# Performance work log

Measured on AMD Instinct MI355X. Metric: run time of the kernel, lower is better.

Reference implementation:

```python
import jax, jax.numpy as jnp
import numpy as np

N = 10000      # nodes
E = 160000     # edges
F_IN = 128     # input_feature
G = 64         # graphs in batch
NC = 10        # num_classes
H1, H2, H3 = 1000, 700, 200


def _xavier(k, fi, fo):
    lim = float(np.sqrt(6.0 / (fi + fo)))
    return jax.random.uniform(k, (fi, fo), jnp.float32, -lim, lim)


def setup_inputs() -> dict:
    key = jax.random.key(0)
    ks = jax.random.split(key, 8)
    x = jax.random.normal(ks[0], (N, F_IN), jnp.float32)
    edge_index = jax.random.randint(ks[1], (2, E), 0, N)
    batch = jnp.sort(jax.random.randint(ks[2], (N,), 0, G))
    return {
        "x": x,
        "edge_index": edge_index,
        "batch": batch,
        "W1": _xavier(ks[3], F_IN, H1), "b1": jnp.zeros((H1,), jnp.float32),
        "W2": _xavier(ks[4], H1, H2),   "b2": jnp.zeros((H2,), jnp.float32),
        "W3": _xavier(ks[5], H2, H3),   "b3": jnp.zeros((H3,), jnp.float32),
        "Wl": _xavier(ks[6], H3, NC),   "bl": jnp.zeros((NC,), jnp.float32),
    }


def _gcn_conv(x, W, b, src, dst, dinv):
    # GCNConv: h = xW; out_i = sum_{j->i} d_j^-1/2 d_i^-1/2 h_j + d_i^-1 h_i + b
    h = x @ W
    coef = dinv[src] * dinv[dst]                      # [E]
    agg = jax.ops.segment_sum(h[src] * coef[:, None], dst, num_segments=N)
    agg = agg + h * (dinv * dinv)[:, None]            # self-loop term
    return agg + b


def reference(x, edge_index, batch, W1, b1, W2, b2, W3, b3, Wl, bl):
    src, dst = edge_index[0], edge_index[1]
    # degree with self-loops (edge weight 1), computed on target nodes
    deg = jax.ops.segment_sum(jnp.ones((E,), x.dtype), dst, num_segments=N) + 1.0
    dinv = jax.lax.rsqrt(deg)

    h = jax.nn.relu(_gcn_conv(x, W1, b1, src, dst, dinv))
    h = jax.nn.relu(_gcn_conv(h, W2, b2, src, dst, dinv))
    h = jax.nn.relu(_gcn_conv(h, W3, b3, src, dst, dinv))

    # global_mean_pool over graph ids
    s = jax.ops.segment_sum(h, batch, num_segments=G)
    cnt = jax.ops.segment_sum(jnp.ones((N,), h.dtype), batch, num_segments=G)
    pooled = s / jnp.maximum(cnt, 1.0)[:, None]

    # dropout is identity in eval mode
    return pooled @ Wl + bl
```

## Files before the change

### kernel.cpp

```cpp
#include <hip/hip_runtime.h>
#include <hip/hip_bf16.h>
#include <stdint.h>


#define SLOT 64

__device__ __forceinline__ uint16_t f2b(float f) {
    union { float f; uint32_t u; } v; v.f = f;
    return (uint16_t)((v.u + 0x7fffu + ((v.u >> 16) & 1u)) >> 16);
}
__device__ __forceinline__ float blo(uint32_t u) { union { uint32_t u; float f; } v; v.u = u << 16; return v.f; }
__device__ __forceinline__ float bhi(uint32_t u) { union { uint32_t u; float f; } v; v.u = u & 0xffff0000u; return v.f; }

__global__ void k_scatter(const int* __restrict__ src, const int* __restrict__ dst,
                          int* __restrict__ cursor, int* __restrict__ slots, int E) {
    int e = blockIdx.x * blockDim.x + threadIdx.x;
    if (e < E) {
        int s = src[e], d = dst[e];
        int pos = atomicAdd(&cursor[d], 1);
        if (pos < SLOT) slots[d * SLOT + pos] = s;
    }
}

__global__ void k_prep(const float* __restrict__ W1, const float* __restrict__ W2,
                       const float* __restrict__ W3,
                       uint16_t* __restrict__ T1, uint16_t* __restrict__ T2,
                       uint16_t* __restrict__ T3,
                       const float* __restrict__ b1, const float* __restrict__ b2,
                       const float* __restrict__ b3,
                       float* __restrict__ p1, float* __restrict__ p2,
                       float* __restrict__ p3,
                       const float* __restrict__ x, uint16_t* __restrict__ xb,
                       const int* __restrict__ deg, float* __restrict__ dinv,
                       int N, int F, int H1, int H2, int H3,
                       int Fp, int H1p, int H2p, int H3p, int n8) {
    __shared__ float tile[32][33];
    int z = blockIdx.z;
    if (z < 3) {
        const float* W; uint16_t* T; int K, Nn, Kp, Np;
        if (z == 0)      { W = W1; T = T1; K = F;  Nn = H1; Kp = Fp;  Np = H1p; }
        else if (z == 1) { W = W2; T = T2; K = H1; Nn = H2; Kp = H1p; Np = H2p; }
        else             { W = W3; T = T3; K = H2; Nn = H3; Kp = H2p; Np = H3p; }
        if ((int)blockIdx.x * 32 >= Kp || (int)blockIdx.y * 32 >= Np) return;
        int k0 = blockIdx.x * 32, n0 = blockIdx.y * 32;
        int tx = threadIdx.x, ty = threadIdx.y;
        for (int i = ty; i < 32; i += 8) {
            int k = k0 + i, n = n0 + tx;
            tile[i][tx] = (k < K && n < Nn) ? W[(size_t)k * Nn + n] : 0.f;
        }
        __syncthreads();
        for (int i = ty; i < 32; i += 8) {
            int n = n0 + i, k = k0 + tx;
            T[(size_t)n * Kp + k] = f2b(tile[tx][i]);
        }
    } else {
        int id = (blockIdx.y * gridDim.x + blockIdx.x) * 256 + threadIdx.y * 32 + threadIdx.x;
        if (z == 3) {
            if (id < H1p) p1[id] = (id < H1) ? b1[id] : 0.f;
            else if (id < H1p + H2p) { int k = id - H1p; p2[k] = (k < H2) ? b2[k] : 0.f; }
            else if (id < H1p + H2p + H3p) { int k = id - H1p - H2p; p3[k] = (k < H3) ? b3[k] : 0.f; }
        } else if (z == 4) {
            if (id < n8) {
                const float4* x4 = (const float4*)x;
                float4 a = x4[2 * id], b = x4[2 * id + 1];
                uint4 o;
                o.x = (uint32_t)f2b(a.x) | ((uint32_t)f2b(a.y) << 16);
                o.y = (uint32_t)f2b(a.z) | ((uint32_t)f2b(a.w) << 16);
                o.z = (uint32_t)f2b(b.x) | ((uint32_t)f2b(b.y) << 16);
                o.w = (uint32_t)f2b(b.z) | ((uint32_t)f2b(b.w) << 16);
                ((uint4*)xb)[id] = o;
            }
        } else {
            if (id < N) dinv[id] = rsqrtf((float)deg[id] + 1.0f);
        }
    }
}

__global__ __launch_bounds__(256) void k_agg_panel(
    const uint16_t* __restrict__ in, uint16_t* __restrict__ out,
    const int* __restrict__ deg_, const int* __restrict__ slots,
    const float* __restrict__ dinv, const float* __restrict__ bias,
    int N, int Hc, int HcReal, int padWrite, int pc, int P, int relu) {
    int slotg = blockIdx.x & 7;
    int panel = slotg % P;
    int seg   = slotg / P;
    int nseg  = 8 / P;
    int segLen = (N + nseg - 1) / nseg;
    int wave = threadIdx.x >> 6, lane = threadIdx.x & 63;
    int half = lane >> 5, sub = lane & 31;
    int item = (blockIdx.x >> 3) * 128 + wave * 32 + sub;
    int rel = item / pc;
    if (rel >= segLen) return;
    int node = seg * segLen + rel;
    if (node >= N) return;
    int j = panel * pc + (item - rel * pc);
    if (j >= HcReal) {
        if (padWrite && half == 0)
            ((uint4*)out)[(size_t)node * Hc + j] = (uint4){0u, 0u, 0u, 0u};
        return;
    }
    int deg = deg_[node];
    if (deg > SLOT) deg = SLOT;
    int base = node * SLOT;
    float dv = dinv[node];
    const uint4* in4 = (const uint4*)in;
    float a[8] = {0.f, 0.f, 0.f, 0.f, 0.f, 0.f, 0.f, 0.f};
    if (half == 0) {
        float self = dv * dv;
        uint4 v = in4[(size_t)node * Hc + j];
        a[0] = self * blo(v.x); a[1] = self * bhi(v.x);
        a[2] = self * blo(v.y); a[3] = self * bhi(v.y);
        a[4] = self * blo(v.z); a[5] = self * bhi(v.z);
        a[6] = self * blo(v.w); a[7] = self * bhi(v.w);
    }
    int D8 = deg & ~7;
    int e = 4 * half;
    if (e < D8) {
        int4 q = *(const int4*)&slots[base + e];
        uint4 h0 = in4[(size_t)q.x * Hc + j];
        uint4 h1 = in4[(size_t)q.y * Hc + j];
        uint4 h2 = in4[(size_t)q.z * Hc + j];
        uint4 h3 = in4[(size_t)q.w * Hc + j];
        float c0 = dinv[q.x] * dv, c1 = dinv[q.y] * dv;
        float c2 = dinv[q.z] * dv, c3 = dinv[q.w] * dv;
        for (e += 8; e < D8; e += 8) {
            int4 qn = *(const int4*)&slots[base + e];
            uint4 g0 = in4[(size_t)qn.x * Hc + j];
            uint4 g1 = in4[(size_t)qn.y * Hc + j];
            uint4 g2 = in4[(size_t)qn.z * Hc + j];
            uint4 g3 = in4[(size_t)qn.w * Hc + j];
            float d0 = dinv[qn.x] * dv, d1 = dinv[qn.y] * dv;
            float d2 = dinv[qn.z] * dv, d3 = dinv[qn.w] * dv;
            a[0] += c0 * blo(h0.x); a[1] += c0 * bhi(h0.x);
            a[2] += c0 * blo(h0.y); a[3] += c0 * bhi(h0.y);
            a[4] += c0 * blo(h0.z); a[5] += c0 * bhi(h0.z);
            a[6] += c0 * blo(h0.w); a[7] += c0 * bhi(h0.w);
            a[0] += c1 * blo(h1.x); a[1] += c1 * bhi(h1.x);
            a[2] += c1 * blo(h1.y); a[3] += c1 * bhi(h1.y);
            a[4] += c1 * blo(h1.z); a[5] += c1 * bhi(h1.z);
            a[6] += c1 * blo(h1.w); a[7] += c1 * bhi(h1.w);
            a[0] += c2 * blo(h2.x); a[1] += c2 * bhi(h2.x);
            a[2] += c2 * blo(h2.y); a[3] += c2 * bhi(h2.y);
            a[4] += c2 * blo(h2.z); a[5] += c2 * bhi(h2.z);
            a[6] += c2 * blo(h2.w); a[7] += c2 * bhi(h2.w);
            a[0] += c3 * blo(h3.x); a[1] += c3 * bhi(h3.x);
            a[2] += c3 * blo(h3.y); a[3] += c3 * bhi(h3.y);
            a[4] += c3 * blo(h3.z); a[5] += c3 * bhi(h3.z);
            a[6] += c3 * blo(h3.w); a[7] += c3 * bhi(h3.w);
            h0 = g0; h1 = g1; h2 = g2; h3 = g3;
            c0 = d0; c1 = d1; c2 = d2; c3 = d3;
        }
        a[0] += c0 * blo(h0.x); a[1] += c0 * bhi(h0.x);
        a[2] += c0 * blo(h0.y); a[3] += c0 * bhi(h0.y);
        a[4] += c0 * blo(h0.z); a[5] += c0 * bhi(h0.z);
        a[6] += c0 * blo(h0.w); a[7] += c0 * bhi(h0.w);
        a[0] += c1 * blo(h1.x); a[1] += c1 * bhi(h1.x);
        a[2] += c1 * blo(h1.y); a[3] += c1 * bhi(h1.y);
        a[4] += c1 * blo(h1.z); a[5] += c1 * bhi(h1.z);
        a[6] += c1 * blo(h1.w); a[7] += c1 * bhi(h1.w);
        a[0] += c2 * blo(h2.x); a[1] += c2 * bhi(h2.x);
        a[2] += c2 * blo(h2.y); a[3] += c2 * bhi(h2.y);
        a[4] += c2 * blo(h2.z); a[5] += c2 * bhi(h2.z);
        a[6] += c2 * blo(h2.w); a[7] += c2 * bhi(h2.w);
        a[0] += c3 * blo(h3.x); a[1] += c3 * bhi(h3.x);
        a[2] += c3 * blo(h3.y); a[3] += c3 * bhi(h3.y);
        a[4] += c3 * blo(h3.z); a[5] += c3 * bhi(h3.z);
        a[6] += c3 * blo(h3.w); a[7] += c3 * bhi(h3.w);
    }
    int t0 = half ? (D8 + 4 < deg ? D8 + 4 : deg) : D8;
    int t1 = half ? deg : (D8 + 4 < deg ? D8 + 4 : deg);
    for (int ee = t0; ee < t1; ++ee) {
        int s0 = slots[base + ee];
        uint4 h = in4[(size_t)s0 * Hc + j];
        float c = dinv[s0] * dv;
        a[0] += c * blo(h.x); a[1] += c * bhi(h.x);
        a[2] += c * blo(h.y); a[3] += c * bhi(h.y);
        a[4] += c * blo(h.z); a[5] += c * bhi(h.z);
        a[6] += c * blo(h.w); a[7] += c * bhi(h.w);
    }
#pragma unroll
    for (int t = 0; t < 8; ++t) a[t] += __shfl_xor(a[t], 32, 64);
    if (half == 0) {
        if (bias) {
            const float4* b4 = (const float4*)bias;
            float4 b0 = b4[2 * j], b1 = b4[2 * j + 1];
            a[0] += b0.x; a[1] += b0.y; a[2] += b0.z; a[3] += b0.w;
            a[4] += b1.x; a[5] += b1.y; a[6] += b1.z; a[7] += b1.w;
        }
        if (relu) {
#pragma unroll
            for (int t = 0; t < 8; ++t) a[t] = fmaxf(a[t], 0.f);
        }
        uint4 o;
        o.x = (uint32_t)f2b(a[0]) | ((uint32_t)f2b(a[1]) << 16);
        o.y = (uint32_t)f2b(a[2]) | ((uint32_t)f2b(a[3]) << 16);
        o.z = (uint32_t)f2b(a[4]) | ((uint32_t)f2b(a[5]) << 16);
        o.w = (uint32_t)f2b(a[6]) | ((uint32_t)f2b(a[7]) << 16);
        ((uint4*)out)[(size_t)node * Hc + j] = o;
    }
}

__global__ __launch_bounds__(256) void k_pool_fast(
    const uint16_t* __restrict__ h, const int* __restrict__ batch,
    float* __restrict__ pooled_sum, int N, int H, int Hp) {
    int j    = threadIdx.x & 63;
    int slot = threadIdx.x >> 6;
    int Hc   = H >> 2;
    if (j >= Hc) return;
    int HcP  = Hp >> 2;
    const uint2* h2 = (const uint2*)h;
    int base = (blockIdx.x * 4 + slot) * 16;
    float a0 = 0.f, a1 = 0.f, a2 = 0.f, a3 = 0.f;
    int gcur = -1;
#pragma unroll 4
    for (int t = 0; t < 16; ++t) {
        int node = base + t;
        if (node < N) {
            int g = batch[node];
            if (g != gcur) {
                if (gcur >= 0) {
                    float* ps = &pooled_sum[(size_t)gcur * H + j * 4];
                    atomicAdd(&ps[0], a0); atomicAdd(&ps[1], a1);
                    atomicAdd(&ps[2], a2); atomicAdd(&ps[3], a3);
                }
                gcur = g; a0 = a1 = a2 = a3 = 0.f;
            }
            uint2 v = h2[(size_t)node * HcP + j];
            a0 += blo(v.x); a1 += bhi(v.x);
            a2 += blo(v.y); a3 += bhi(v.y);
        }
    }
    if (gcur >= 0) {
        float* ps = &pooled_sum[(size_t)gcur * H + j * 4];
        atomicAdd(&ps[0], a0); atomicAdd(&ps[1], a1);
        atomicAdd(&ps[2], a2); atomicAdd(&ps[3], a3);
    }
}

typedef __attribute__((ext_vector_type(8))) short short8;
typedef __attribute__((ext_vector_type(4))) float floatx4;

#define LDSP(p) ((__attribute__((address_space(3))) void*)(uintptr_t)(p))
#define GLBP(p) ((const __attribute__((address_space(1))) void*)(uintptr_t)(p))

__global__ __launch_bounds__(256) void k_gemm128(
    const uint16_t* __restrict__ A, const uint16_t* __restrict__ Bt,
    const float* __restrict__ bias, uint16_t* __restrict__ Cout,
    int M, int Kp, int Np, int relu, int nrg, int nr) {
    int bid = blockIdx.x;
    int rsub = bid & 7;
    int t_ = bid >> 3;
    int rg = t_ % nrg, cc = t_ / nrg;
    int rt = rg * 8 + rsub;
    if (rt >= nr) return;
    int row0 = rt * 128, col0 = cc * 128;

    __shared__ uint16_t As[128 * 64];
    __shared__ uint16_t Bs[128 * 64];
    int tid = threadIdx.x;
    int wave = tid >> 6, lane = tid & 63;
    int quad = lane >> 4, m16 = lane & 15;
    int wr = wave >> 1, wc = wave & 1;

    int rA = tid >> 3;
    int cA = (tid & 7) ^ (rA & 7);
    const uint16_t* gA = A  + (size_t)(row0 + rA) * Kp + cA * 8;
    const uint16_t* gB = Bt + (size_t)(col0 + rA) * Kp + cA * 8;
    uint16_t* lA = As + tid * 8;
    uint16_t* lB = Bs + tid * 8;
    size_t rowStep32 = (size_t)32 * Kp;

    floatx4 acc[4][4];
#pragma unroll
    for (int i = 0; i < 4; ++i)
#pragma unroll
        for (int j = 0; j < 4; ++j) acc[i][j] = (floatx4){0.f, 0.f, 0.f, 0.f};

    const short* Ash = (const short*)As;
    const short* Bsh = (const short*)Bs;
    int swA = m16 & 7;

    for (int k0 = 0; k0 < Kp; k0 += 64) {
#pragma unroll
        for (int p = 0; p < 4; ++p) {
            __builtin_amdgcn_global_load_lds(GLBP(gA + p * rowStep32), LDSP(lA + p * 2048), 16, 0, 0);
            __builtin_amdgcn_global_load_lds(GLBP(gB + p * rowStep32), LDSP(lB + p * 2048), 16, 0, 0);
        }
        gA += 64; gB += 64;
        __syncthreads();
#pragma unroll
        for (int h = 0; h < 2; ++h) {
            short8 af[4], bf[4];
            int c = h * 4 + quad;
            int pos = (c ^ swA) * 8;
#pragma unroll
            for (int i = 0; i < 4; ++i)
                af[i] = *(const short8*)&Ash[(wr * 64 + i * 16 + m16) * 64 + pos];
#pragma unroll
            for (int j = 0; j < 4; ++j)
                bf[j] = *(const short8*)&Bsh[(wc * 64 + j * 16 + m16) * 64 + pos];
#pragma unroll
            for (int i = 0; i < 4; ++i)
#pragma unroll
                for (int j = 0; j < 4; ++j)
                    acc[i][j] = __builtin_amdgcn_mfma_f32_16x16x32_bf16(af[i], bf[j], acc[i][j], 0, 0, 0);
        }
        __syncthreads();
    }

    float bv[4];
#pragma unroll
    for (int j = 0; j < 4; ++j) {
        int n = col0 + wc * 64 + j * 16 + m16;
        bv[j] = bias ? bias[n] : 0.f;
    }
#pragma unroll
    for (int i = 0; i < 4; ++i) {
        int mBase = row0 + wr * 64 + i * 16 + quad * 4;
#pragma unroll
        for (int r = 0; r < 4; ++r) {
            int m = mBase + r;
            if (m < M) {
#pragma unroll
                for (int j = 0; j < 4; ++j) {
                    int n = col0 + wc * 64 + j * 16 + m16;
                    float v = acc[i][j][r] + bv[j];
                    if (relu) v = fmaxf(v, 0.f);
                    Cout[(size_t)m * Np + n] = f2b(v);
                }
            }
        }
    }
}

__global__ __launch_bounds__(256) void k_gemm64(
    const uint16_t* __restrict__ A, const uint16_t* __restrict__ Bt,
    const float* __restrict__ bias, uint16_t* __restrict__ Cout,
    int M, int Kp, int Np, int relu, int nrg, int nr) {
    int bid = blockIdx.x;
    int rsub = bid & 7;
    int t_ = bid >> 3;
    int rg = t_ % nrg, cc = t_ / nrg;
    int rt = rg * 8 + rsub;
    if (rt >= nr) return;
    int row0 = rt * 128, col0 = cc * 64;

    __shared__ uint16_t As[128 * 64];
    __shared__ uint16_t Bs[64 * 64];
    int tid = threadIdx.x;
    int wave = tid >> 6, lane = tid & 63;
    int quad = lane >> 4, m16 = lane & 15;
    int wr = wave >> 1, wc = wave & 1;

    int rA = tid >> 3;
    int cA = (tid & 7) ^ (rA & 7);
    const uint16_t* gA = A  + (size_t)(row0 + rA) * Kp + cA * 8;
    const uint16_t* gB = Bt + (size_t)(col0 + rA) * Kp + cA * 8;
    uint16_t* lA = As + tid * 8;
    uint16_t* lB = Bs + tid * 8;
    size_t rowStep32 = (size_t)32 * Kp;

    floatx4 acc[4][2];
#pragma unroll
    for (int i = 0; i < 4; ++i)
#pragma unroll
        for (int j = 0; j < 2; ++j) acc[i][j] = (floatx4){0.f, 0.f, 0.f, 0.f};

    const short* Ash = (const short*)As;
    const short* Bsh = (const short*)Bs;
    int swA = m16 & 7;

    for (int k0 = 0; k0 < Kp; k0 += 64) {
#pragma unroll
        for (int p = 0; p < 4; ++p)
            __builtin_amdgcn_global_load_lds(GLBP(gA + p * rowStep32), LDSP(lA + p * 2048), 16, 0, 0);
#pragma unroll
        for (int p = 0; p < 2; ++p)
            __builtin_amdgcn_global_load_lds(GLBP(gB + p * rowStep32), LDSP(lB + p * 2048), 16, 0, 0);
        gA += 64; gB += 64;
        __syncthreads();
#pragma unroll
        for (int h = 0; h < 2; ++h) {
            short8 af[4], bf[2];
            int c = h * 4 + quad;
            int pos = (c ^ swA) * 8;
#pragma unroll
            for (int i = 0; i < 4; ++i)
                af[i] = *(const short8*)&Ash[(wr * 64 + i * 16 + m16) * 64 + pos];
#pragma unroll
            for (int j = 0; j < 2; ++j)
                bf[j] = *(const short8*)&Bsh[(wc * 32 + j * 16 + m16) * 64 + pos];
#pragma unroll
            for (int i = 0; i < 4; ++i)
#pragma unroll
                for (int j = 0; j < 2; ++j)
                    acc[i][j] = __builtin_amdgcn_mfma_f32_16x16x32_bf16(af[i], bf[j], acc[i][j], 0, 0, 0);
        }
        __syncthreads();
    }

    float bv[2];
#pragma unroll
    for (int j = 0; j < 2; ++j) {
        int n = col0 + wc * 32 + j * 16 + m16;
        bv[j] = bias ? bias[n] : 0.f;
    }
#pragma unroll
    for (int i = 0; i < 4; ++i) {
        int mBase = row0 + wr * 64 + i * 16 + quad * 4;
#pragma unroll
        for (int r = 0; r < 4; ++r) {
            int m = mBase + r;
            if (m < M) {
#pragma unroll
                for (int j = 0; j < 2; ++j) {
                    int n = col0 + wc * 32 + j * 16 + m16;
                    float v = acc[i][j][r] + bv[j];
                    if (relu) v = fmaxf(v, 0.f);
                    Cout[(size_t)m * Np + n] = f2b(v);
                }
            }
        }
    }
}

__global__ void k_classifier(const float* __restrict__ pooled_sum,
                             const int* __restrict__ batch,
                             const float* __restrict__ Wl, const float* __restrict__ bl,
                             float* __restrict__ out, int N, int H, int NC) {
    int g = blockIdx.x, c = threadIdx.x;
    int lo = 0, hi = N;
    while (lo < hi) { int mid = (lo + hi) >> 1; if (batch[mid] < g) lo = mid + 1; else hi = mid; }
    int start = lo;
    lo = start; hi = N;
    while (lo < hi) { int mid = (lo + hi) >> 1; if (batch[mid] < g + 1) lo = mid + 1; else hi = mid; }
    int end = lo;
    float scale = 1.0f / fmaxf((float)(end - start), 1.0f);
    if (c < NC) {
        float acc = 0.f;
        for (int k = 0; k < H; ++k) acc += pooled_sum[(size_t)g * H + k] * Wl[(size_t)k * NC + c];
        out[(size_t)g * NC + c] = acc * scale + bl[c];
    }
}

static inline size_t align256(size_t x) { return (x + 255) & ~(size_t)255; }
static inline int pad128(int x) { return (x + 127) & ~127; }

extern "C" void kernel_launch(void* const* d_in, const int* in_sizes, int n_in,
                              void* d_out, int out_size, void* d_ws, size_t ws_size,
                              hipStream_t stream) {
    const float* x   = (const float*)d_in[0];
    const int*   ei  = (const int*)d_in[1];
    const int*   bat = (const int*)d_in[2];
    const float* W1  = (const float*)d_in[3];
    const float* b1  = (const float*)d_in[4];
    const float* W2  = (const float*)d_in[5];
    const float* b2  = (const float*)d_in[6];
    const float* W3  = (const float*)d_in[7];
    const float* b3  = (const float*)d_in[8];
    const float* Wl  = (const float*)d_in[9];
    const float* bl  = (const float*)d_in[10];

    const int N  = in_sizes[2];
    const int E  = in_sizes[1] / 2;
    const int F  = in_sizes[0] / N;
    const int H1 = in_sizes[4];
    const int H2 = in_sizes[6];
    const int H3 = in_sizes[8];
    const int NC = in_sizes[10];
    const int G  = out_size / NC;
    const int* src = ei;
    const int* dst = ei + E;

    const int Mp  = pad128(N);
    const int Fp  = F;
    const int H1p = pad128(H1);
    const int H2p = pad128(H2);
    const int H3p = pad128(H3);
    const int Hc2real = (H2 + 7) / 8;
    const int Hc3real = (H3 + 7) / 8;

    char* p = (char*)d_ws;
    size_t off = 0;
    auto carve = [&](size_t bytes) { void* q = p + off; off += align256(bytes); return q; };
    uint16_t* xb     = (uint16_t*)carve((size_t)Mp * Fp * 2);
    uint16_t* bufA   = (uint16_t*)carve((size_t)Mp * 2048);
    uint16_t* bufB   = (uint16_t*)carve((size_t)Mp * 2048);
    uint16_t* W1t    = (uint16_t*)carve((size_t)H1p * Fp * 2);
    uint16_t* W2t    = (uint16_t*)carve((size_t)H2p * H1p * 2);
    uint16_t* W3t    = (uint16_t*)carve((size_t)H3p * H2p * 2);
    float* b1p       = (float*)carve((size_t)H1p * 4);
    float* b2p       = (float*)carve((size_t)H2p * 4);
    float* b3p       = (float*)carve((size_t)H3p * 4);
    float* dinv      = (float*)carve((size_t)N * 4);
    int*   cursor    = (int*)carve((size_t)N * 4);
    float* pooled    = (float*)carve((size_t)G * H3 * 4);
    int*   slots     = (int*)carve((size_t)N * SLOT * 4);
    (void)ws_size;

    const int nbE = (E + 255) / 256;

    size_t zlen = (size_t)((char*)pooled - (char*)cursor) + (size_t)G * H3 * 4;
    hipMemsetAsync(cursor, 0, zlen, stream);

    k_scatter<<<nbE, 256, 0, stream>>>(src, dst, cursor, slots, E);

    k_prep<<<dim3(32, 32, 6), dim3(32, 8), 0, stream>>>(
        W1, W2, W3, W1t, W2t, W3t, b1, b2, b3, b1p, b2p, b3p, x, xb,
        cursor, dinv, N, F, H1, H2, H3, Fp, H1p, H2p, H3p, N * F / 8);

    auto agg_grid = [&](int P, int pc) {
        int nseg = 8 / P;
        int segLen = (N + nseg - 1) / nseg;
        return 8 * ((segLen * pc + 127) / 128);
    };

    const int nr  = Mp / 128;
    const int nrg = (nr + 7) / 8;

    k_agg_panel<<<agg_grid(1, 16), 256, 0, stream>>>(
        xb, bufA, cursor, slots, dinv, nullptr, N, 16, 16, 0, 16, 1, 0);
    k_gemm128<<<nrg * 8 * (H1p / 128), 256, 0, stream>>>(
        bufA, W1t, b1p, bufB, N, Fp, H1p, 1, nrg, nr);

    k_gemm128<<<nrg * 8 * (H2p / 128), 256, 0, stream>>>(
        bufB, W2t, nullptr, bufA, N, H1p, H2p, 0, nrg, nr);
    k_agg_panel<<<agg_grid(8, 12), 256, 0, stream>>>(
        bufA, bufB, cursor, slots, dinv, b2p, N, 96, Hc2real, 1, 12, 8, 1);

    k_gemm64<<<nrg * 8 * (H3p / 64), 256, 0, stream>>>(
        bufB, W3t, nullptr, bufA, N, H2p, H3p, 0, nrg, nr);
    k_agg_panel<<<agg_grid(4, 8), 256, 0, stream>>>(
        bufA, bufB, cursor, slots, dinv, b3p, N, 32, Hc3real, 0, 8, 4, 1);

    k_pool_fast<<<(N + 63) / 64, 256, 0, stream>>>(
        (const uint16_t*)bufB, bat, pooled, N, H3, H3p);
    k_classifier<<<G, 64, 0, stream>>>(pooled, bat, Wl, bl, (float*)d_out, N, H3, NC);
}
```

Before: 238.5 us.

## Fold edge scatter into prep kernel, compute dinv inline, fuse pool with classifier

Moves the edge-scatter pass into the z-slice of the prep kernel that previously computed dinv. The aggregation kernels now recompute the normalization coefficient with rsqrtf from the degree counts, so the separate dinv array is gone. Pooling and the classifier are merged through a last-block-done atomic counter. Together these remove two kernel launches and one dependency pass. The cost is extra rsqrt work per edge and a serial classifier tail that runs in a single block.

Result: slower. 308.2 us (+29.2%).

```diff
diff --git a/kernel.cpp b/kernel.cpp
--- a/kernel.cpp
+++ b/kernel.cpp
@@ -11,16 +11,6 @@
 }
 __device__ __forceinline__ float blo(uint32_t u) { union { uint32_t u; float f; } v; v.u = u << 16; return v.f; }
 __device__ __forceinline__ float bhi(uint32_t u) { union { uint32_t u; float f; } v; v.u = u & 0xffff0000u; return v.f; }
-
-__global__ void k_scatter(const int* __restrict__ src, const int* __restrict__ dst,
-                          int* __restrict__ cursor, int* __restrict__ slots, int E) {
-    int e = blockIdx.x * blockDim.x + threadIdx.x;
-    if (e < E) {
-        int s = src[e], d = dst[e];
-        int pos = atomicAdd(&cursor[d], 1);
-        if (pos < SLOT) slots[d * SLOT + pos] = s;
-    }
-}
 
 __global__ void k_prep(const float* __restrict__ W1, const float* __restrict__ W2,
                        const float* __restrict__ W3,
@@ -31,8 +21,9 @@
                        float* __restrict__ p1, float* __restrict__ p2,
                        float* __restrict__ p3,
                        const float* __restrict__ x, uint16_t* __restrict__ xb,
-                       const int* __restrict__ deg, float* __restrict__ dinv,
-                       int N, int F, int H1, int H2, int H3,
+                       const int* __restrict__ src, const int* __restrict__ dst,
+                       int* __restrict__ cursor, int* __restrict__ slots, int E,
+                       int F, int H1, int H2, int H3,
                        int Fp, int H1p, int H2p, int H3p, int n8) {
     __shared__ float tile[32][33];
     int z = blockIdx.z;
@@ -71,15 +62,19 @@
                 ((uint4*)xb)[id] = o;
             }
         } else {
-            if (id < N) dinv[id] = rsqrtf((float)deg[id] + 1.0f);
+            if (id < E) {
+                int s = src[id], d = dst[id];
+                int pos = atomicAdd(&cursor[d], 1);
+                if (pos < SLOT) slots[d * SLOT + pos] = s;
+            }
         }
     }
 }
 
 __global__ __launch_bounds__(256) void k_agg_panel(
     const uint16_t* __restrict__ in, uint16_t* __restrict__ out,
-    const int* __restrict__ deg_, const int* __restrict__ slots,
-    const float* __restrict__ dinv, const float* __restrict__ bias,
+    const int* __restrict__ degt, const int* __restrict__ slots,
+    const float* __restrict__ bias,
     int N, int Hc, int HcReal, int padWrite, int pc, int P, int relu) {
     int slotg = blockIdx.x & 7;
     int panel = slotg % P;
@@ -99,14 +94,14 @@
             ((uint4*)out)[(size_t)node * Hc + j] = (uint4){0u, 0u, 0u, 0u};
         return;
     }
-    int deg = deg_[node];
-    if (deg > SLOT) deg = SLOT;
+    int degFull = degt[node];
+    int deg = degFull > SLOT ? SLOT : degFull;
     int base = node * SLOT;
-    float dv = dinv[node];
+    float ndf = (float)(degFull + 1);
     const uint4* in4 = (const uint4*)in;
     float a[8] = {0.f, 0.f, 0.f, 0.f, 0.f, 0.f, 0.f, 0.f};
     if (half == 0) {
-        float self = dv * dv;
+        float self = 1.0f / ndf;
         uint4 v = in4[(size_t)node * Hc + j];
         a[0] = self * blo(v.x); a[1] = self * bhi(v.x);
         a[2] = self * blo(v.y); a[3] = self * bhi(v.y);
@@ -121,16 +116,20 @@
         uint4 h1 = in4[(size_t)q.y * Hc + j];
         uint4 h2 = in4[(size_t)q.z * Hc + j];
         uint4 h3 = in4[(size_t)q.w * Hc + j];
-        float c0 = dinv[q.x] * dv, c1 = dinv[q.y] * dv;
-        float c2 = dinv[q.z] * dv, c3 = dinv[q.w] * dv;
+        float c0 = rsqrtf(ndf * (float)(degt[q.x] + 1));
+        float c1 = rsqrtf(ndf * (float)(degt[q.y] + 1));
+        float c2 = rsqrtf(ndf * (float)(degt[q.z] + 1));
+        float c3 = rsqrtf(ndf * (float)(degt[q.w] + 1));
         for (e += 8; e < D8; e += 8) {
             int4 qn = *(const int4*)&slots[base + e];
             uint4 g0 = in4[(size_t)qn.x * Hc + j];
             uint4 g1 = in4[(size_t)qn.y * Hc + j];
             uint4 g2 = in4[(size_t)qn.z * Hc + j];
             uint4 g3 = in4[(size_t)qn.w * Hc + j];
-            float d0 = dinv[qn.x] * dv, d1 = dinv[qn.y] * dv;
-            float d2 = dinv[qn.z] * dv, d3 = dinv[qn.w] * dv;
+            float d0 = rsqrtf(ndf * (float)(degt[qn.x] + 1));
+            float d1 = rsqrtf(ndf * (float)(degt[qn.y] + 1));
+            float d2 = rsqrtf(ndf * (float)(degt[qn.z] + 1));
+            float d3 = rsqrtf(ndf * (float)(degt[qn.w] + 1));
             a[0] += c0 * blo(h0.x); a[1] += c0 * bhi(h0.x);
             a[2] += c0 * blo(h0.y); a[3] += c0 * bhi(h0.y);
             a[4] += c0 * blo(h0.z); a[5] += c0 * bhi(h0.z);
@@ -172,7 +171,7 @@
     for (int ee = t0; ee < t1; ++ee) {
         int s0 = slots[base + ee];
         uint4 h = in4[(size_t)s0 * Hc + j];
-        float c = dinv[s0] * dv;
+        float c = rsqrtf(ndf * (float)(degt[s0] + 1));
         a[0] += c * blo(h.x); a[1] += c * bhi(h.x);
         a[2] += c * blo(h.y); a[3] += c * bhi(h.y);
         a[4] += c * blo(h.z); a[5] += c * bhi(h.z);
@@ -200,40 +199,70 @@
     }
 }
 
-__global__ __launch_bounds__(256) void k_pool_fast(
+__global__ __launch_bounds__(256) void k_pool_cls(
     const uint16_t* __restrict__ h, const int* __restrict__ batch,
-    float* __restrict__ pooled_sum, int N, int H, int Hp) {
-    int j    = threadIdx.x & 63;
-    int slot = threadIdx.x >> 6;
+    float* __restrict__ pooled_sum, int* __restrict__ done,
+    const float* __restrict__ Wl, const float* __restrict__ bl,
+    float* __restrict__ out, int N, int H, int Hp, int NC, int G) {
+    int tid = threadIdx.x;
+    int j    = tid & 63;
+    int slot = tid >> 6;
     int Hc   = H >> 2;
-    if (j >= Hc) return;
+    bool act = (j < Hc);
     int HcP  = Hp >> 2;
     const uint2* h2 = (const uint2*)h;
-    int base = (blockIdx.x * 4 + slot) * 16;
-    float a0 = 0.f, a1 = 0.f, a2 = 0.f, a3 = 0.f;
-    int gcur = -1;
+    if (act) {
+        int base = (blockIdx.x * 4 + slot) * 16;
+        float a0 = 0.f, a1 = 0.f, a2 = 0.f, a3 = 0.f;
+        int gcur = -1;
 #pragma unroll 4
-    for (int t = 0; t < 16; ++t) {
-        int node = base + t;
-        if (node < N) {
-            int g = batch[node];
-            if (g != gcur) {
-                if (gcur >= 0) {
-                    float* ps = &pooled_sum[(size_t)gcur * H + j * 4];
-                    atomicAdd(&ps[0], a0); atomicAdd(&ps[1], a1);
-                    atomicAdd(&ps[2], a2); atomicAdd(&ps[3], a3);
+        for (int t = 0; t < 16; ++t) {
+            int node = base + t;
+            if (node < N) {
+                int g = batch[node];
+                if (g != gcur) {
+                    if (gcur >= 0) {
+                        float* ps = &pooled_sum[(size_t)gcur * H + j * 4];
+                        atomicAdd(&ps[0], a0); atomicAdd(&ps[1], a1);
+                        atomicAdd(&ps[2], a2); atomicAdd(&ps[3], a3);
+                    }
+                    gcur = g; a0 = a1 = a2 = a3 = 0.f;
                 }
-                gcur = g; a0 = a1 = a2 = a3 = 0.f;
+                uint2 v = h2[(size_t)node * HcP + j];
+                a0 += blo(v.x); a1 += bhi(v.x);
+                a2 += blo(v.y); a3 += bhi(v.y);
             }
-            uint2 v = h2[(size_t)node * HcP + j];
-            a0 += blo(v.x); a1 += bhi(v.x);
-            a2 += blo(v.y); a3 += bhi(v.y);
-        }
-    }
-    if (gcur >= 0) {
-        float* ps = &pooled_sum[(size_t)gcur * H + j * 4];
-        atomicAdd(&ps[0], a0); atomicAdd(&ps[1], a1);
-        atomicAdd(&ps[2], a2); atomicAdd(&ps[3], a3);
+        }
+        if (gcur >= 0) {
+            float* ps = &pooled_sum[(size_t)gcur * H + j * 4];
+            atomicAdd(&ps[0], a0); atomicAdd(&ps[1], a1);
+            atomicAdd(&ps[2], a2); atomicAdd(&ps[3], a3);
+        }
+    }
+    __syncthreads();
+    __shared__ int lastFlag;
+    if (tid == 0) {
+        __threadfence();
+        int t = atomicAdd(done, 1);
+        lastFlag = (t == (int)gridDim.x - 1) ? 1 : 0;
+    }
+    __syncthreads();
+    if (lastFlag) {
+        __threadfence();
+        for (int idx = tid; idx < G * NC; idx += 256) {
+            int g = idx / NC, c = idx - g * NC;
+            int lo = 0, hi = N;
+            while (lo < hi) { int mid = (lo + hi) >> 1; if (batch[mid] < g) lo = mid + 1; else hi = mid; }
+            int start = lo;
+            lo = start; hi = N;
+            while (lo < hi) { int mid = (lo + hi) >> 1; if (batch[mid] < g + 1) lo = mid + 1; else hi = mid; }
+            int end = lo;
+            float scale = 1.0f / fmaxf((float)(end - start), 1.0f);
+            float acc = 0.f;
+            for (int k = 0; k < H; ++k)
+                acc += pooled_sum[(size_t)g * H + k] * Wl[(size_t)k * NC + c];
+            out[(size_t)g * NC + c] = acc * scale + bl[c];
+        }
     }
 }
 
@@ -421,25 +450,6 @@
                 }
             }
         }
-    }
-}
-
-__global__ void k_classifier(const float* __restrict__ pooled_sum,
-                             const int* __restrict__ batch,
-                             const float* __restrict__ Wl, const float* __restrict__ bl,
-                             float* __restrict__ out, int N, int H, int NC) {
-    int g = blockIdx.x, c = threadIdx.x;
-    int lo = 0, hi = N;
-    while (lo < hi) { int mid = (lo + hi) >> 1; if (batch[mid] < g) lo = mid + 1; else hi = mid; }
-    int start = lo;
-    lo = start; hi = N;
-    while (lo < hi) { int mid = (lo + hi) >> 1; if (batch[mid] < g + 1) lo = mid + 1; else hi = mid; }
-    int end = lo;
-    float scale = 1.0f / fmaxf((float)(end - start), 1.0f);
-    if (c < NC) {
-        float acc = 0.f;
-        for (int k = 0; k < H; ++k) acc += pooled_sum[(size_t)g * H + k] * Wl[(size_t)k * NC + c];
-        out[(size_t)g * NC + c] = acc * scale + bl[c];
     }
 }
 
@@ -492,22 +502,19 @@
     float* b1p       = (float*)carve((size_t)H1p * 4);
     float* b2p       = (float*)carve((size_t)H2p * 4);
     float* b3p       = (float*)carve((size_t)H3p * 4);
-    float* dinv      = (float*)carve((size_t)N * 4);
     int*   cursor    = (int*)carve((size_t)N * 4);
     float* pooled    = (float*)carve((size_t)G * H3 * 4);
+    int*   done      = (int*)carve(4);
     int*   slots     = (int*)carve((size_t)N * SLOT * 4);
     (void)ws_size;
 
-    const int nbE = (E + 255) / 256;
-
-    size_t zlen = (size_t)((char*)pooled - (char*)cursor) + (size_t)G * H3 * 4;
+    size_t zlen = (size_t)((char*)done - (char*)cursor) + 4;
     hipMemsetAsync(cursor, 0, zlen, stream);
-
-    k_scatter<<<nbE, 256, 0, stream>>>(src, dst, cursor, slots, E);
 
     k_prep<<<dim3(32, 32, 6), dim3(32, 8), 0, stream>>>(
         W1, W2, W3, W1t, W2t, W3t, b1, b2, b3, b1p, b2p, b3p, x, xb,
-        cursor, dinv, N, F, H1, H2, H3, Fp, H1p, H2p, H3p, N * F / 8);
+        src, dst, cursor, slots, E,
+        F, H1, H2, H3, Fp, H1p, H2p, H3p, N * F / 8);
 
     auto agg_grid = [&](int P, int pc) {
         int nseg = 8 / P;
@@ -519,21 +526,21 @@
     const int nrg = (nr + 7) / 8;
 
     k_agg_panel<<<agg_grid(1, 16), 256, 0, stream>>>(
-        xb, bufA, cursor, slots, dinv, nullptr, N, 16, 16, 0, 16, 1, 0);
+        xb, bufA, cursor, slots, nullptr, N, 16, 16, 0, 16, 1, 0);
     k_gemm128<<<nrg * 8 * (H1p / 128), 256, 0, stream>>>(
         bufA, W1t, b1p, bufB, N, Fp, H1p, 1, nrg, nr);
 
     k_gemm128<<<nrg * 8 * (H2p / 128), 256, 0, stream>>>(
         bufB, W2t, nullptr, bufA, N, H1p, H2p, 0, nrg, nr);
     k_agg_panel<<<agg_grid(8, 12), 256, 0, stream>>>(
-        bufA, bufB, cursor, slots, dinv, b2p, N, 96, Hc2real, 1, 12, 8, 1);
+        bufA, bufB, cursor, slots, b2p, N, 96, Hc2real, 1, 12, 8, 1);
 
     k_gemm64<<<nrg * 8 * (H3p / 64), 256, 0, stream>>>(
         bufB, W3t, nullptr, bufA, N, H2p, H3p, 0, nrg, nr);
     k_agg_panel<<<agg_grid(4, 8), 256, 0, stream>>>(
-        bufA, bufB, cursor, slots, dinv, b3p, N, 32, Hc3real, 0, 8, 4, 1);
-
-    k_pool_fast<<<(N + 63) / 64, 256, 0, stream>>>(
-        (const uint16_t*)bufB, bat, pooled, N, H3, H3p);
-    k_classifier<<<G, 64, 0, stream>>>(pooled, bat, Wl, bl, (float*)d_out, N, H3, NC);
-}
+        bufA, bufB, cursor, slots, b3p, N, 32, Hc3real, 0, 8, 4, 1);
+
+    k_pool_cls<<<(N + 63) / 64, 256, 0, stream>>>(
+        (const uint16_t*)bufB, bat, pooled, done, Wl, bl, (float*)d_out,
+        N, H3, H3p, NC, G);
+}
```
